# Kernel optimization log

Measured on AMD Instinct MI355X. Metric: run time of the kernel, lower is better.

## Reference

```python
import jax, jax.numpy as jnp
import numpy as np

N = 100000
E = 1600000
IN_FEATS = 128
H_FEATS = 64
BN_EPS = 1e-5


def setup_inputs() -> dict:
    key = jax.random.key(0)
    ks = jax.random.split(key, 8)
    features = jax.random.normal(ks[0], (N, IN_FEATS), dtype=jnp.float32)
    src = jax.random.randint(ks[1], (E,), 0, N, dtype=jnp.int32)
    dst = jax.random.randint(ks[2], (E,), 0, N, dtype=jnp.int32)
    # GraphConv weights (Glorot-ish scale) and biases
    W1 = jax.random.normal(ks[3], (IN_FEATS, H_FEATS), dtype=jnp.float32) / np.sqrt(IN_FEATS)
    b1 = jnp.zeros((H_FEATS,), dtype=jnp.float32)
    W2 = jax.random.normal(ks[4], (H_FEATS, H_FEATS), dtype=jnp.float32) / np.sqrt(H_FEATS)
    b2 = jnp.zeros((H_FEATS,), dtype=jnp.float32)
    gamma1 = jnp.ones((H_FEATS,), dtype=jnp.float32)
    beta1 = jnp.zeros((H_FEATS,), dtype=jnp.float32)
    gamma2 = jnp.ones((H_FEATS,), dtype=jnp.float32)
    beta2 = jnp.zeros((H_FEATS,), dtype=jnp.float32)
    return {"features": features, "W1": W1, "b1": b1, "gamma1": gamma1,
            "beta1": beta1, "W2": W2, "b2": b2, "gamma2": gamma2,
            "beta2": beta2, "src": src, "dst": dst}


def _degrees(src, dst):
    ones = jnp.ones((E,), dtype=jnp.float32)
    deg_out = jax.ops.segment_sum(ones, src, num_segments=N)
    deg_in = jax.ops.segment_sum(ones, dst, num_segments=N)
    # DGL clamps degree to >= 1 to avoid div by zero
    norm_src = jax.lax.rsqrt(jnp.maximum(deg_out, 1.0))  # [N]
    norm_dst = jax.lax.rsqrt(jnp.maximum(deg_in, 1.0))   # [N]
    return norm_src, norm_dst


def _graph_conv(x, W, b, src, dst, norm_src, norm_dst):
    # norm='both': D_out^{-1/2} scaling on src, sum-aggregate, D_in^{-1/2} on dst
    h = x * norm_src[:, None]          # [N, in]
    h = h @ W                          # [N, out] (transform before aggregate)
    msgs = h[src]                      # [E, out] gather
    agg = jax.ops.segment_sum(msgs, dst, num_segments=N)  # [N, out] scatter-add
    out = agg * norm_dst[:, None] + b
    return jax.nn.elu(out)


def _batch_norm(x, gamma, beta):
    mean = jnp.mean(x, axis=0)
    var = jnp.mean(jnp.square(x - mean), axis=0)
    return (x - mean) * jax.lax.rsqrt(var + BN_EPS) * gamma + beta


def reference(features, W1, b1, gamma1, beta1, W2, b2, gamma2, beta2, src, dst):
    # dropout p=0.0 (eval) -> identity
    norm_src, norm_dst = _degrees(src, dst)
    h1 = _graph_conv(features, W1, b1, src, dst, norm_src, norm_dst)
    h1 = _batch_norm(h1, gamma1, beta1)
    h2 = _graph_conv(h1, W2, b2, src, dst, norm_src, norm_dst)
    h2 = _batch_norm(h2, gamma2, beta2)
    return h2
```

## Files before the change

### kernel.cpp

```cpp
#include <hip/hip_runtime.h>
#include <cmath>

#define NFEAT_IN 128
#define NFEAT_H 64
#define BN_EPS 1e-5f
#define SCAP 2560

typedef unsigned short ushort_t;
typedef unsigned int uint_t;
typedef __attribute__((ext_vector_type(8))) short short8v;
typedef __attribute__((ext_vector_type(4))) float f32x4;

__device__ inline float b2f(ushort_t u) {
    return __uint_as_float(((uint_t)u) << 16);
}

__device__ inline ushort_t f2b(float f) {
    uint_t x = __float_as_uint(f);
    return (ushort_t)((x + 0x7FFFu + ((x >> 16) & 1u)) >> 16);
}


__global__ __launch_bounds__(256) void deg_s_kernel(const int* __restrict__ src,
                                                    int* __restrict__ deg_s, int E) {
    int i = blockIdx.x * 256 + threadIdx.x;
    if (i < E) atomicAdd(&deg_s[src[i]], 1);
}

__global__ __launch_bounds__(256) void dst_append_kernel(const int* __restrict__ src,
                                                         const int* __restrict__ dst,
                                                         int* __restrict__ curD,
                                                         uint_t* __restrict__ dbuf, int E) {
    int e = blockIdx.x * 256 + threadIdx.x;
    if (e < E) {
        int s = src[e], d = dst[e];
        int pD = atomicAdd(&curD[(d >> 7) * 16], 1);
        if (pD < SCAP) dbuf[(long long)(d >> 7) * SCAP + pD] = ((uint_t)s << 7) | (uint_t)(d & 127);
    }
}

__global__ __launch_bounds__(256) void bucket_hist_kernel(const uint_t* __restrict__ dbuf,
                                                          const int* __restrict__ curD,
                                                          int* __restrict__ deg_d, int N) {
    __shared__ int hist[128];
    int bb = blockIdx.x;
    int t = threadIdx.x;
    if (t < 128) hist[t] = 0;
    __syncthreads();
    int cnt = curD[bb * 16];
    if (cnt > SCAP) cnt = SCAP;
    long long base = (long long)bb * SCAP;
    for (int i = t; i < cnt; i += 256) atomicAdd(&hist[dbuf[base + i] & 127], 1);
    __syncthreads();
    if (t < 128) {
        int node = bb * 128 + t;
        if (node < N) deg_d[node] = hist[t];
    }
}

__global__ __launch_bounds__(256) void norm_scan_kernel(const int* __restrict__ deg_s,
                                                        const int* __restrict__ deg_d,
                                                        float* __restrict__ norm_s,
                                                        float* __restrict__ norm_d,
                                                        int* __restrict__ start,
                                                        int* __restrict__ counter,
                                                        float* __restrict__ stats, int N) {
    int tid = threadIdx.x;
    int i = blockIdx.x * 256 + tid;
    if (blockIdx.x == 0 && tid < 128) stats[tid] = 0.f;
    int lane = tid & 63, w = tid >> 6;
    int ds = 0, dd = 0;
    if (i < N) { ds = deg_s[i]; dd = deg_d[i]; }
    int pd = (dd + 7) & ~7;

    int x = pd;
#pragma unroll
    for (int off = 1; off < 64; off <<= 1) {
        int y = __shfl_up(x, off, 64);
        if (lane >= off) x += y;
    }
    __shared__ int wsum[4];
    __shared__ int blockbase;
    if (lane == 63) wsum[w] = x;
    __syncthreads();
    if (tid == 0)
        blockbase = atomicAdd(counter, wsum[0] + wsum[1] + wsum[2] + wsum[3]);
    __syncthreads();
    int base = blockbase;
    for (int ww = 0; ww < w; ++ww) base += wsum[ww];
    int st = base + x - pd;

    if (i < N) {
        norm_s[i] = rsqrtf((float)(ds > 1 ? ds : 1));
        norm_d[i] = rsqrtf((float)(dd > 1 ? dd : 1));
        start[i] = st;
    }
}

__global__ __launch_bounds__(256) void bucket_scatter_kernel(const uint_t* __restrict__ dbuf,
                                                             const int* __restrict__ curD,
                                                             const int* __restrict__ start,
                                                             int* __restrict__ col, int N) {
    __shared__ int cur[128];
    __shared__ int sst[128];
    int b = blockIdx.x, t = threadIdx.x;
    if (t < 128) {
        cur[t] = 0;
        int node = b * 128 + t;
        sst[t] = (node < N) ? start[node] : 0;
    }
    __syncthreads();
    int cnt = curD[b * 16];
    if (cnt > SCAP) cnt = SCAP;
    long long base = (long long)b * SCAP;
    for (int i = t; i < cnt; i += 256) {
        uint_t p = dbuf[base + i];
        int d0 = (int)(p & 127u);
        int s = (int)(p >> 7);
        int off = atomicAdd(&cur[d0], 1);
        col[sst[d0] + off] = s;
    }
}


__global__ __launch_bounds__(256) void gemm1_mfma(const float* __restrict__ x,
                                                  const float* __restrict__ W,
                                                  const float* __restrict__ norm,
                                                  ushort_t* __restrict__ out, int n) {
    constexpr int K = 128;
    __shared__ ushort_t sWh[64 * K];
    __shared__ ushort_t sWl[64 * K];
    int tid = threadIdx.x;
    for (int i = tid; i < K * 64; i += 256) {
        int k = i >> 6, f = i & 63;
        float v = W[i];
        ushort_t hi = f2b(v);
        ushort_t lo = f2b(v - b2f(hi));
        int idx = f * K + (((k >> 3) ^ (f & 7)) << 3) + (k & 7);
        sWh[idx] = hi;
        sWl[idx] = lo;
    }
    int w = tid >> 6, l = tid & 63, g = l >> 4;
    int rA = blockIdx.x * 64 + w * 16 + (l & 15);
    f32x4 acc[4];
#pragma unroll
    for (int nt = 0; nt < 4; ++nt) acc[nt] = (f32x4){0.f, 0.f, 0.f, 0.f};
    __syncthreads();

#pragma unroll
    for (int ks = 0; ks < K / 32; ++ks) {
        float av[8];
        if (rA < n) {
            const float* px = x + (long long)rA * K + ks * 32 + g * 8;
            float4 p0 = *(const float4*)px;
            float4 p1 = *(const float4*)(px + 4);
            av[0] = p0.x; av[1] = p0.y; av[2] = p0.z; av[3] = p0.w;
            av[4] = p1.x; av[5] = p1.y; av[6] = p1.z; av[7] = p1.w;
        } else {
#pragma unroll
            for (int j = 0; j < 8; ++j) av[j] = 0.f;
        }
        short8v ah, al;
#pragma unroll
        for (int j = 0; j < 8; ++j) {
            ushort_t h = f2b(av[j]);
            ah[j] = (short)h;
            al[j] = (short)f2b(av[j] - b2f(h));
        }
#pragma unroll
        for (int nt = 0; nt < 4; ++nt) {
            int f = nt * 16 + (l & 15);
            int c = (ks * 4 + g) ^ (f & 7);
            short8v bh = *(const short8v*)&sWh[f * K + (c << 3)];
            short8v bl = *(const short8v*)&sWl[f * K + (c << 3)];
            acc[nt] = __builtin_amdgcn_mfma_f32_16x16x32_bf16(ah, bh, acc[nt], 0, 0, 0);
            acc[nt] = __builtin_amdgcn_mfma_f32_16x16x32_bf16(ah, bl, acc[nt], 0, 0, 0);
            acc[nt] = __builtin_amdgcn_mfma_f32_16x16x32_bf16(al, bh, acc[nt], 0, 0, 0);
        }
    }
    int rb = blockIdx.x * 64 + w * 16 + g * 4;
    float nv[4];
#pragma unroll
    for (int j = 0; j < 4; ++j) {
        int r = rb + j;
        nv[j] = (r < n) ? norm[r] : 0.f;
    }
#pragma unroll
    for (int nt = 0; nt < 4; ++nt) {
        int cc = nt * 16 + (l & 15);
#pragma unroll
        for (int j = 0; j < 4; ++j) {
            int r = rb + j;
            if (r < n) out[(long long)r * 64 + cc] = f2b(acc[nt][j] * nv[j]);
        }
    }
}

__global__ __launch_bounds__(256) void gemm2_mfma(const ushort_t* __restrict__ x,
                                                  const float* __restrict__ W,
                                                  const float* __restrict__ coef,
                                                  const float* __restrict__ biasK,
                                                  const float* __restrict__ norm,
                                                  ushort_t* __restrict__ out, int n) {
    constexpr int K = 64;
    __shared__ ushort_t sWh[64 * K];
    __shared__ ushort_t sWl[64 * K];
    int tid = threadIdx.x;
    for (int i = tid; i < K * 64; i += 256) {
        int k = i >> 6, f = i & 63;
        float v = coef[k] * W[i];
        ushort_t hi = f2b(v);
        ushort_t lo = f2b(v - b2f(hi));
        int idx = f * K + (((k >> 3) ^ (f & 7)) << 3) + (k & 7);
        sWh[idx] = hi;
        sWl[idx] = lo;
    }
    int w = tid >> 6, l = tid & 63, g = l >> 4;
    int rA = blockIdx.x * 64 + w * 16 + (l & 15);
    f32x4 acc[4];
#pragma unroll
    for (int nt = 0; nt < 4; ++nt) acc[nt] = (f32x4){0.f, 0.f, 0.f, 0.f};
    __syncthreads();

#pragma unroll
    for (int ks = 0; ks < 2; ++ks) {
        short8v ah;
        if (rA < n) {
            uint4 u = *(const uint4*)(x + (long long)rA * 64 + ks * 32 + g * 8);
            union { uint4 u; short8v s; } cvt;
            cvt.u = u;
            ah = cvt.s;
        } else {
#pragma unroll
            for (int j = 0; j < 8; ++j) ah[j] = 0;
        }
#pragma unroll
        for (int nt = 0; nt < 4; ++nt) {
            int f = nt * 16 + (l & 15);
            int c = (ks * 4 + g) ^ (f & 7);
            short8v bh = *(const short8v*)&sWh[f * K + (c << 3)];
            short8v bl = *(const short8v*)&sWl[f * K + (c << 3)];
            acc[nt] = __builtin_amdgcn_mfma_f32_16x16x32_bf16(ah, bh, acc[nt], 0, 0, 0);
            acc[nt] = __builtin_amdgcn_mfma_f32_16x16x32_bf16(ah, bl, acc[nt], 0, 0, 0);
        }
    }
    int rb = blockIdx.x * 64 + w * 16 + g * 4;
    float nv[4];
#pragma unroll
    for (int j = 0; j < 4; ++j) {
        int r = rb + j;
        nv[j] = (r < n) ? norm[r] : 0.f;
    }
#pragma unroll
    for (int nt = 0; nt < 4; ++nt) {
        int cc = nt * 16 + (l & 15);
        float bk = biasK[cc];
#pragma unroll
        for (int j = 0; j < 4; ++j) {
            int r = rb + j;
            if (r < n) out[(long long)r * 64 + cc] = f2b((acc[nt][j] + bk) * nv[j]);
        }
    }
}

__global__ __launch_bounds__(256) void agg_fused_kernel(const ushort_t* __restrict__ h,
                                                        const int* __restrict__ start,
                                                        const int* __restrict__ degd,
                                                        const int* __restrict__ col,
                                                        const float* __restrict__ normd,
                                                        const float* __restrict__ bias,
                                                        ushort_t* __restrict__ outp,
                                                        float* __restrict__ stats, int N) {
    int tid = threadIdx.x;
    int w = tid >> 6;
    int lane = tid & 63;
    int g = lane >> 3;
    int j = lane & 7;

    float bb[8];
#pragma unroll
    for (int i = 0; i < 8; ++i) bb[i] = bias[j * 8 + i];

    float sum[8], sq[8];
#pragma unroll
    for (int i = 0; i < 8; ++i) { sum[i] = 0.f; sq[i] = 0.f; }

    for (int node = blockIdx.x * 4 + w; node < N; node += gridDim.x * 4) {
        int s0 = start[node];
        int d = degd[node];
        float acc[8];
#pragma unroll
        for (int i = 0; i < 8; ++i) acc[i] = 0.f;

        int k = 0;
        for (; k + 16 <= d; k += 16) {
            int c0 = col[s0 + k + g];
            int c1 = col[s0 + k + 8 + g];
            uint4 a = ((const uint4*)(h + (long long)c0 * 64))[j];
            uint4 b = ((const uint4*)(h + (long long)c1 * 64))[j];
            acc[0] += __uint_as_float(a.x << 16);
            acc[1] += __uint_as_float(a.x & 0xFFFF0000u);
            acc[2] += __uint_as_float(a.y << 16);
            acc[3] += __uint_as_float(a.y & 0xFFFF0000u);
            acc[4] += __uint_as_float(a.z << 16);
            acc[5] += __uint_as_float(a.z & 0xFFFF0000u);
            acc[6] += __uint_as_float(a.w << 16);
            acc[7] += __uint_as_float(a.w & 0xFFFF0000u);
            acc[0] += __uint_as_float(b.x << 16);
            acc[1] += __uint_as_float(b.x & 0xFFFF0000u);
            acc[2] += __uint_as_float(b.y << 16);
            acc[3] += __uint_as_float(b.y & 0xFFFF0000u);
            acc[4] += __uint_as_float(b.z << 16);
            acc[5] += __uint_as_float(b.z & 0xFFFF0000u);
            acc[6] += __uint_as_float(b.w << 16);
            acc[7] += __uint_as_float(b.w & 0xFFFF0000u);
        }
        for (; k + 8 <= d; k += 8) {
            int c0 = col[s0 + k + g];
            uint4 a = ((const uint4*)(h + (long long)c0 * 64))[j];
            acc[0] += __uint_as_float(a.x << 16);
            acc[1] += __uint_as_float(a.x & 0xFFFF0000u);
            acc[2] += __uint_as_float(a.y << 16);
            acc[3] += __uint_as_float(a.y & 0xFFFF0000u);
            acc[4] += __uint_as_float(a.z << 16);
            acc[5] += __uint_as_float(a.z & 0xFFFF0000u);
            acc[6] += __uint_as_float(a.w << 16);
            acc[7] += __uint_as_float(a.w & 0xFFFF0000u);
        }
        if (k < d) {
            int idx = k + g;
            if (idx < d) {
                int c0 = col[s0 + idx];
                uint4 a = ((const uint4*)(h + (long long)c0 * 64))[j];
                acc[0] += __uint_as_float(a.x << 16);
                acc[1] += __uint_as_float(a.x & 0xFFFF0000u);
                acc[2] += __uint_as_float(a.y << 16);
                acc[3] += __uint_as_float(a.y & 0xFFFF0000u);
                acc[4] += __uint_as_float(a.z << 16);
                acc[5] += __uint_as_float(a.z & 0xFFFF0000u);
                acc[6] += __uint_as_float(a.w << 16);
                acc[7] += __uint_as_float(a.w & 0xFFFF0000u);
            }
        }

#pragma unroll
        for (int i = 0; i < 8; ++i) {
            acc[i] += __shfl_xor(acc[i], 8, 64);
            acc[i] += __shfl_xor(acc[i], 16, 64);
            acc[i] += __shfl_xor(acc[i], 32, 64);
        }

        if (g == 0) {
            float nv = normd[node];
            float v[8];
#pragma unroll
            for (int i = 0; i < 8; ++i) {
                float t = acc[i] * nv + bb[i];
                t = t > 0.f ? t : expm1f(t);
                v[i] = t;
                sum[i] += t;
                sq[i] += t * t;
            }
            uint4 p;
            p.x = ((uint_t)f2b(v[1]) << 16) | f2b(v[0]);
            p.y = ((uint_t)f2b(v[3]) << 16) | f2b(v[2]);
            p.z = ((uint_t)f2b(v[5]) << 16) | f2b(v[4]);
            p.w = ((uint_t)f2b(v[7]) << 16) | f2b(v[6]);
            ((uint4*)(outp + (long long)node * 64))[j] = p;
        }
    }

    __shared__ float ssum[4][64];
    __shared__ float ssq[4][64];
    if (g == 0) {
#pragma unroll
        for (int i = 0; i < 8; ++i) {
            ssum[w][j * 8 + i] = sum[i];
            ssq[w][j * 8 + i] = sq[i];
        }
    }
    __syncthreads();
    if (tid < 64) {
        float s = ssum[0][tid] + ssum[1][tid] + ssum[2][tid] + ssum[3][tid];
        float q = ssq[0][tid] + ssq[1][tid] + ssq[2][tid] + ssq[3][tid];
        atomicAdd(&stats[tid], s);
        atomicAdd(&stats[64 + tid], q);
    }
}

__global__ __launch_bounds__(64) void bn_fin2_kernel(float* __restrict__ stats,
                                                     const float* __restrict__ gamma,
                                                     const float* __restrict__ beta,
                                                     const float* __restrict__ W2,
                                                     float* __restrict__ coef,
                                                     float* __restrict__ biasK, float inv_n) {
    int f = threadIdx.x;
    float mean = stats[f] * inv_n;
    float var = stats[64 + f] * inv_n - mean * mean;
    float a = gamma[f] * rsqrtf(var + BN_EPS);
    float cB = beta[f] - mean * a;
    coef[f] = a;
    coef[64 + f] = cB;
    stats[f] = 0.f;
    stats[64 + f] = 0.f;
    __shared__ float scB[64];
    scB[f] = cB;
    __syncthreads();
    float s = 0.f;
    for (int k = 0; k < 64; ++k) s = fmaf(scB[k], W2[k * 64 + f], s);
    biasK[f] = s;
}

__global__ __launch_bounds__(64) void bn_finalize(float* __restrict__ stats,
                                                  const float* __restrict__ gamma,
                                                  const float* __restrict__ beta,
                                                  float* __restrict__ coef, float inv_n) {
    int f = threadIdx.x;
    float mean = stats[f] * inv_n;
    float var = stats[64 + f] * inv_n - mean * mean;
    float a = gamma[f] * rsqrtf(var + BN_EPS);
    coef[f] = a;
    coef[64 + f] = beta[f] - mean * a;
}

__global__ __launch_bounds__(256) void bn_apply_b2f(const uint4* __restrict__ in,
                                                    const float* __restrict__ coef,
                                                    float4* __restrict__ out, long long n4) {
    long long i = (long long)blockIdx.x * 256 + threadIdx.x;
    if (i >= n4) return;
    int k = (int)((i & 7) << 3);
    uint4 u = in[i];
    float4 a, b;
    a.x = __uint_as_float(u.x << 16) * coef[k] + coef[64 + k];
    a.y = __uint_as_float(u.x & 0xFFFF0000u) * coef[k + 1] + coef[64 + k + 1];
    a.z = __uint_as_float(u.y << 16) * coef[k + 2] + coef[64 + k + 2];
    a.w = __uint_as_float(u.y & 0xFFFF0000u) * coef[k + 3] + coef[64 + k + 3];
    b.x = __uint_as_float(u.z << 16) * coef[k + 4] + coef[64 + k + 4];
    b.y = __uint_as_float(u.z & 0xFFFF0000u) * coef[k + 5] + coef[64 + k + 5];
    b.z = __uint_as_float(u.w << 16) * coef[k + 6] + coef[64 + k + 6];
    b.w = __uint_as_float(u.w & 0xFFFF0000u) * coef[k + 7] + coef[64 + k + 7];
    out[i * 2] = a;
    out[i * 2 + 1] = b;
}


extern "C" void kernel_launch(void* const* d_in, const int* in_sizes, int n_in,
                              void* d_out, int out_size, void* d_ws, size_t ws_size,
                              hipStream_t stream) {
    const float* features = (const float*)d_in[0];
    const float* W1 = (const float*)d_in[1];
    const float* b1 = (const float*)d_in[2];
    const float* gamma1 = (const float*)d_in[3];
    const float* beta1 = (const float*)d_in[4];
    const float* W2 = (const float*)d_in[5];
    const float* b2 = (const float*)d_in[6];
    const float* gamma2 = (const float*)d_in[7];
    const float* beta2 = (const float*)d_in[8];
    const int* src = (const int*)d_in[9];
    const int* dst = (const int*)d_in[10];
    int N = in_sizes[0] / NFEAT_IN;
    int E = in_sizes[9];

    float inv_n = 1.0f / (float)N;
    long long tot = (long long)N * 64;
    int eblk256 = (E + 255) / 256;
    int nblk256 = (N + 255) / 256;
    int NB = (N + 127) >> 7;
    int gblk = (N + 63) / 64;
    long long n4 = (long long)N * 8;
    int a4blk = (int)((n4 + 255) / 256);

    long long bufcap = (long long)NB * SCAP;
    long long colcap = (long long)E + 8LL * N;
    long long int_total = (16LL * NB + 4 + 3LL * N + bufcap + colcap + 3) & ~3LL;
    long long flt_count = ((2LL * N + 128 + 128 + 64) + 3) & ~3LL;

    int* ip = (int*)d_ws;
    int* curD = ip;
    int* counter = ip + 16LL * NB;
    int* deg_s = ip + 16LL * NB + 4;
    int* deg_d = deg_s + N;
    int* startv = deg_d + N;
    uint_t* dbuf = (uint_t*)(startv + N);
    int* col = (int*)(dbuf + bufcap);
    float* fp = (float*)(ip + int_total);
    float* norm_s = fp;
    float* norm_d = fp + N;
    float* stats = fp + 2LL * N;
    float* coef = stats + 128;
    float* biasK = coef + 128;
    ushort_t* hA = (ushort_t*)(fp + flt_count);
    ushort_t* oB = hA + tot;

    hipMemsetAsync(curD, 0, sizeof(int) * (16LL * NB + 4 + N), stream);
    deg_s_kernel<<<eblk256, 256, 0, stream>>>(src, deg_s, E);
    dst_append_kernel<<<eblk256, 256, 0, stream>>>(src, dst, curD, dbuf, E);
    bucket_hist_kernel<<<NB, 256, 0, stream>>>(dbuf, curD, deg_d, N);
    norm_scan_kernel<<<nblk256, 256, 0, stream>>>(deg_s, deg_d, norm_s, norm_d,
                                                  startv, counter, stats, N);
    bucket_scatter_kernel<<<NB, 256, 0, stream>>>(dbuf, curD, startv, col, N);

    gemm1_mfma<<<gblk, 256, 0, stream>>>(features, W1, norm_s, hA, N);
    agg_fused_kernel<<<2048, 256, 0, stream>>>(hA, startv, deg_d, col, norm_d, b1,
                                               oB, stats, N);
    bn_fin2_kernel<<<1, 64, 0, stream>>>(stats, gamma1, beta1, W2, coef, biasK, inv_n);

    gemm2_mfma<<<gblk, 256, 0, stream>>>(oB, W2, coef, biasK, norm_s, hA, N);
    agg_fused_kernel<<<2048, 256, 0, stream>>>(hA, startv, deg_d, col, norm_d, b2,
                                               oB, stats, N);
    bn_finalize<<<1, 64, 0, stream>>>(stats, gamma2, beta2, coef, inv_n);
    bn_apply_b2f<<<a4blk, 256, 0, stream>>>((const uint4*)oB, coef, (float4*)d_out, n4);
}
```

Baseline: 476.8 us.

## Split layer-1 aggregation into four source-range phases for gather cache locality

Edges in each destination's adjacency list are sorted into four groups by source-node quarter, with per-node group counts stored. Layer-1 aggregation then runs as four passes, each gathering only from one quarter of the feature table, so the working set of gathered rows fits better in cache. A separate finalize kernel applies normalization, bias, ELU and the BN statistics. The cost is extra passes that round-trip the accumulator through bf16 memory, which adds traffic and a rounding step per pass. The separate degree-count kernel is also fused into the append kernel.

```diff
diff --git a/kernel.cpp b/kernel.cpp
--- a/kernel.cpp
+++ b/kernel.cpp
@@ -21,19 +21,15 @@
 }
 
 
-__global__ __launch_bounds__(256) void deg_s_kernel(const int* __restrict__ src,
-                                                    int* __restrict__ deg_s, int E) {
-    int i = blockIdx.x * 256 + threadIdx.x;
-    if (i < E) atomicAdd(&deg_s[src[i]], 1);
-}
-
-__global__ __launch_bounds__(256) void dst_append_kernel(const int* __restrict__ src,
+__global__ __launch_bounds__(256) void deg_append_kernel(const int* __restrict__ src,
                                                          const int* __restrict__ dst,
+                                                         int* __restrict__ deg_s,
                                                          int* __restrict__ curD,
                                                          uint_t* __restrict__ dbuf, int E) {
     int e = blockIdx.x * 256 + threadIdx.x;
     if (e < E) {
         int s = src[e], d = dst[e];
+        atomicAdd(&deg_s[s], 1);
         int pD = atomicAdd(&curD[(d >> 7) * 16], 1);
         if (pD < SCAP) dbuf[(long long)(d >> 7) * SCAP + pD] = ((uint_t)s << 7) | (uint_t)(d & 127);
     }
@@ -97,28 +93,49 @@
     }
 }
 
-__global__ __launch_bounds__(256) void bucket_scatter_kernel(const uint_t* __restrict__ dbuf,
-                                                             const int* __restrict__ curD,
-                                                             const int* __restrict__ start,
-                                                             int* __restrict__ col, int N) {
-    __shared__ int cur[128];
-    __shared__ int sst[128];
+__global__ __launch_bounds__(256) void bucket_scatter2_kernel(const uint_t* __restrict__ dbuf,
+                                                              const int* __restrict__ curD,
+                                                              const int* __restrict__ start,
+                                                              int* __restrict__ col,
+                                                              uint2* __restrict__ rcnt,
+                                                              int N, int Q) {
+    __shared__ int cnt4[128][4];
+    __shared__ int cur[128][4];
     int b = blockIdx.x, t = threadIdx.x;
-    if (t < 128) {
-        cur[t] = 0;
-        int node = b * 128 + t;
-        sst[t] = (node < N) ? start[node] : 0;
-    }
+    if (t < 128) { cnt4[t][0] = 0; cnt4[t][1] = 0; cnt4[t][2] = 0; cnt4[t][3] = 0; }
     __syncthreads();
     int cnt = curD[b * 16];
     if (cnt > SCAP) cnt = SCAP;
     long long base = (long long)b * SCAP;
+    int Q2 = 2 * Q, Q3 = 3 * Q;
     for (int i = t; i < cnt; i += 256) {
         uint_t p = dbuf[base + i];
         int d0 = (int)(p & 127u);
         int s = (int)(p >> 7);
-        int off = atomicAdd(&cur[d0], 1);
-        col[sst[d0] + off] = s;
+        int r = (s >= Q) + (s >= Q2) + (s >= Q3);
+        atomicAdd(&cnt4[d0][r], 1);
+    }
+    __syncthreads();
+    if (t < 128) {
+        int node = b * 128 + t;
+        int st = (node < N) ? start[node] : 0;
+        int c0 = cnt4[t][0], c1 = cnt4[t][1], c2 = cnt4[t][2], c3 = cnt4[t][3];
+        cur[t][0] = st;
+        cur[t][1] = st + c0;
+        cur[t][2] = st + c0 + c1;
+        cur[t][3] = st + c0 + c1 + c2;
+        if (node < N)
+            rcnt[node] = make_uint2((uint_t)c0 | ((uint_t)c1 << 16),
+                                    (uint_t)c2 | ((uint_t)c3 << 16));
+    }
+    __syncthreads();
+    for (int i = t; i < cnt; i += 256) {
+        uint_t p = dbuf[base + i];
+        int d0 = (int)(p & 127u);
+        int s = (int)(p >> 7);
+        int r = (s >= Q) + (s >= Q2) + (s >= Q3);
+        int off = atomicAdd(&cur[d0][r], 1);
+        col[off] = s;
     }
 }
 
@@ -260,6 +277,123 @@
             int r = rb + j;
             if (r < n) out[(long long)r * 64 + cc] = f2b((acc[nt][j] + bk) * nv[j]);
         }
+    }
+}
+
+template <bool FIRST>
+__global__ __launch_bounds__(256) void agg_phase_kernel(const ushort_t* __restrict__ h,
+                                                        const int* __restrict__ start,
+                                                        const uint2* __restrict__ rcnt,
+                                                        const int* __restrict__ col,
+                                                        ushort_t* __restrict__ acc,
+                                                        int N, int r) {
+    int tid = threadIdx.x;
+    int w = tid >> 6;
+    int lane = tid & 63;
+    int g = lane >> 3;
+    int j = lane & 7;
+
+    for (int node = blockIdx.x * 4 + w; node < N; node += gridDim.x * 4) {
+        uint2 rc = rcnt[node];
+        int c0 = (int)(rc.x & 0xFFFFu), c1 = (int)(rc.x >> 16);
+        int c2 = (int)(rc.y & 0xFFFFu), c3 = (int)(rc.y >> 16);
+        int s0 = start[node];
+        int cnt;
+        if (r == 0) { cnt = c0; }
+        else if (r == 1) { s0 += c0; cnt = c1; }
+        else if (r == 2) { s0 += c0 + c1; cnt = c2; }
+        else { s0 += c0 + c1 + c2; cnt = c3; }
+        if (!FIRST && cnt == 0) continue;
+
+        float a8[8];
+#pragma unroll
+        for (int i = 0; i < 8; ++i) a8[i] = 0.f;
+
+        int k = 0;
+        for (; k + 8 <= cnt; k += 8) {
+            int c = col[s0 + k + g];
+            uint4 a = ((const uint4*)(h + (long long)c * 64))[j];
+            a8[0] += __uint_as_float(a.x << 16);
+            a8[1] += __uint_as_float(a.x & 0xFFFF0000u);
+            a8[2] += __uint_as_float(a.y << 16);
+            a8[3] += __uint_as_float(a.y & 0xFFFF0000u);
+            a8[4] += __uint_as_float(a.z << 16);
+            a8[5] += __uint_as_float(a.z & 0xFFFF0000u);
+            a8[6] += __uint_as_float(a.w << 16);
+            a8[7] += __uint_as_float(a.w & 0xFFFF0000u);
+        }
+        if (k < cnt) {
+            int idx = k + g;
+            if (idx < cnt) {
+                int c = col[s0 + idx];
+                uint4 a = ((const uint4*)(h + (long long)c * 64))[j];
+                a8[0] += __uint_as_float(a.x << 16);
+                a8[1] += __uint_as_float(a.x & 0xFFFF0000u);
+                a8[2] += __uint_as_float(a.y << 16);
+                a8[3] += __uint_as_float(a.y & 0xFFFF0000u);
+                a8[4] += __uint_as_float(a.z << 16);
+                a8[5] += __uint_as_float(a.z & 0xFFFF0000u);
+                a8[6] += __uint_as_float(a.w << 16);
+                a8[7] += __uint_as_float(a.w & 0xFFFF0000u);
+            }
+        }
+
+#pragma unroll
+        for (int i = 0; i < 8; ++i) {
+            a8[i] += __shfl_xor(a8[i], 8, 64);
+            a8[i] += __shfl_xor(a8[i], 16, 64);
+            a8[i] += __shfl_xor(a8[i], 32, 64);
+        }
+
+        if (g == 0) {
+            uint4* ap = (uint4*)(acc + (long long)node * 64) + j;
+            if (!FIRST) {
+                uint4 o = *ap;
+                a8[0] += __uint_as_float(o.x << 16);
+                a8[1] += __uint_as_float(o.x & 0xFFFF0000u);
+                a8[2] += __uint_as_float(o.y << 16);
+                a8[3] += __uint_as_float(o.y & 0xFFFF0000u);
+                a8[4] += __uint_as_float(o.z << 16);
+                a8[5] += __uint_as_float(o.z & 0xFFFF0000u);
+                a8[6] += __uint_as_float(o.w << 16);
+                a8[7] += __uint_as_float(o.w & 0xFFFF0000u);
+            }
+            uint4 p;
+            p.x = ((uint_t)f2b(a8[1]) << 16) | f2b(a8[0]);
+            p.y = ((uint_t)f2b(a8[3]) << 16) | f2b(a8[2]);
+            p.z = ((uint_t)f2b(a8[5]) << 16) | f2b(a8[4]);
+            p.w = ((uint_t)f2b(a8[7]) << 16) | f2b(a8[6]);
+            *ap = p;
+        }
+    }
+}
+
+__global__ __launch_bounds__(256) void finalize1_kernel(ushort_t* __restrict__ acc,
+                                                        const float* __restrict__ normd,
+                                                        const float* __restrict__ bias,
+                                                        float* __restrict__ stats, int N) {
+    int tid = threadIdx.x;
+    int f = tid & 63;
+    int w = tid >> 6;
+    float b = bias[f];
+    float sum = 0.f, sq = 0.f;
+    for (int node = blockIdx.x * 4 + w; node < N; node += gridDim.x * 4) {
+        long long i = (long long)node * 64 + f;
+        float v = b2f(acc[i]) * normd[node] + b;
+        v = v > 0.f ? v : expm1f(v);
+        acc[i] = f2b(v);
+        sum += v;
+        sq += v * v;
+    }
+    __shared__ float ssum[256], ssq[256];
+    ssum[tid] = sum;
+    ssq[tid] = sq;
+    __syncthreads();
+    if (tid < 64) {
+        float s = ssum[tid] + ssum[tid + 64] + ssum[tid + 128] + ssum[tid + 192];
+        float q = ssq[tid] + ssq[tid + 64] + ssq[tid + 128] + ssq[tid + 192];
+        atomicAdd(&stats[tid], s);
+        atomicAdd(&stats[64 + tid], q);
     }
 }
 
@@ -467,12 +601,13 @@
     int nblk256 = (N + 255) / 256;
     int NB = (N + 127) >> 7;
     int gblk = (N + 63) / 64;
+    int Q = (N + 3) / 4;
     long long n4 = (long long)N * 8;
     int a4blk = (int)((n4 + 255) / 256);
 
     long long bufcap = (long long)NB * SCAP;
     long long colcap = (long long)E + 8LL * N;
-    long long int_total = (16LL * NB + 4 + 3LL * N + bufcap + colcap + 3) & ~3LL;
+    long long int_total = (16LL * NB + 4 + 5LL * N + bufcap + colcap + 3) & ~3LL;
     long long flt_count = ((2LL * N + 128 + 128 + 64) + 3) & ~3LL;
 
     int* ip = (int*)d_ws;
@@ -481,7 +616,8 @@
     int* deg_s = ip + 16LL * NB + 4;
     int* deg_d = deg_s + N;
     int* startv = deg_d + N;
-    uint_t* dbuf = (uint_t*)(startv + N);
+    uint2* rcnt = (uint2*)(startv + N);
+    uint_t* dbuf = (uint_t*)(startv + N + 2LL * N);
     int* col = (int*)(dbuf + bufcap);
     float* fp = (float*)(ip + int_total);
     float* norm_s = fp;
@@ -493,16 +629,18 @@
     ushort_t* oB = hA + tot;
 
     hipMemsetAsync(curD, 0, sizeof(int) * (16LL * NB + 4 + N), stream);
-    deg_s_kernel<<<eblk256, 256, 0, stream>>>(src, deg_s, E);
-    dst_append_kernel<<<eblk256, 256, 0, stream>>>(src, dst, curD, dbuf, E);
+    deg_append_kernel<<<eblk256, 256, 0, stream>>>(src, dst, deg_s, curD, dbuf, E);
     bucket_hist_kernel<<<NB, 256, 0, stream>>>(dbuf, curD, deg_d, N);
     norm_scan_kernel<<<nblk256, 256, 0, stream>>>(deg_s, deg_d, norm_s, norm_d,
                                                   startv, counter, stats, N);
-    bucket_scatter_kernel<<<NB, 256, 0, stream>>>(dbuf, curD, startv, col, N);
+    bucket_scatter2_kernel<<<NB, 256, 0, stream>>>(dbuf, curD, startv, col, rcnt, N, Q);
 
     gemm1_mfma<<<gblk, 256, 0, stream>>>(features, W1, norm_s, hA, N);
-    agg_fused_kernel<<<2048, 256, 0, stream>>>(hA, startv, deg_d, col, norm_d, b1,
-                                               oB, stats, N);
+    agg_phase_kernel<true><<<2048, 256, 0, stream>>>(hA, startv, rcnt, col, oB, N, 0);
+    agg_phase_kernel<false><<<2048, 256, 0, stream>>>(hA, startv, rcnt, col, oB, N, 1);
+    agg_phase_kernel<false><<<2048, 256, 0, stream>>>(hA, startv, rcnt, col, oB, N, 2);
+    agg_phase_kernel<false><<<2048, 256, 0, stream>>>(hA, startv, rcnt, col, oB, N, 3);
+    finalize1_kernel<<<2048, 256, 0, stream>>>(oB, norm_d, b1, stats, N);
     bn_fin2_kernel<<<1, 64, 0, stream>>>(stats, gamma1, beta1, W2, coef, biasK, inv_n);
 
     gemm2_mfma<<<gblk, 256, 0, stream>>>(oB, W2, coef, biasK, norm_s, hA, N);
```

New measurement: 574.7 us. 20.5% more time.

## Fuse degree count into dst bucketing with block-local shared-memory reservation

Applied to the files above, without the earlier changes.

Merges the source-degree atomic pass into the destination bucketing kernel. Each block processes 4096 edges, builds a per-bucket histogram in shared memory, then reserves space in each global bucket with one atomic per bucket instead of one per edge. Positions inside a bucket come from shared-memory atomics. This cuts global atomic contention on the bucket counters and removes one launch and one read of src, at the cost of reading dst twice per block and running fewer, larger blocks.

```diff
diff --git a/kernel.cpp b/kernel.cpp
--- a/kernel.cpp
+++ b/kernel.cpp
@@ -5,6 +5,8 @@
 #define NFEAT_H 64
 #define BN_EPS 1e-5f
 #define SCAP 2560
+#define EPB 4096
+#define NBMAX 800
 
 typedef unsigned short ushort_t;
 typedef unsigned int uint_t;
@@ -21,19 +23,44 @@
 }
 
 
-__global__ __launch_bounds__(256) void deg_s_kernel(const int* __restrict__ src,
-                                                    int* __restrict__ deg_s, int E) {
-    int i = blockIdx.x * 256 + threadIdx.x;
-    if (i < E) atomicAdd(&deg_s[src[i]], 1);
-}
-
-__global__ __launch_bounds__(256) void dst_append_kernel(const int* __restrict__ src,
+__global__ __launch_bounds__(256) void block_append_kernel(const int* __restrict__ src,
+                                                           const int* __restrict__ dst,
+                                                           int* __restrict__ deg_s,
+                                                           int* __restrict__ curD,
+                                                           uint_t* __restrict__ dbuf,
+                                                           int E, int NB) {
+    __shared__ int lcnt[NBMAX];
+    __shared__ int lcur[NBMAX];
+    int t = threadIdx.x;
+    int e0 = blockIdx.x * EPB;
+    int e1 = min(e0 + EPB, E);
+    for (int i = t; i < NB; i += 256) lcnt[i] = 0;
+    __syncthreads();
+    for (int e = e0 + t; e < e1; e += 256)
+        atomicAdd(&lcnt[dst[e] >> 7], 1);
+    __syncthreads();
+    for (int i = t; i < NB; i += 256) {
+        int c = lcnt[i];
+        lcur[i] = (c > 0) ? atomicAdd(&curD[i * 16], c) : 0;
+    }
+    __syncthreads();
+    for (int e = e0 + t; e < e1; e += 256) {
+        int s = src[e], d = dst[e];
+        atomicAdd(&deg_s[s], 1);
+        int pos = atomicAdd(&lcur[d >> 7], 1);
+        if (pos < SCAP) dbuf[(long long)(d >> 7) * SCAP + pos] = ((uint_t)s << 7) | (uint_t)(d & 127);
+    }
+}
+
+__global__ __launch_bounds__(256) void deg_append_kernel(const int* __restrict__ src,
                                                          const int* __restrict__ dst,
+                                                         int* __restrict__ deg_s,
                                                          int* __restrict__ curD,
                                                          uint_t* __restrict__ dbuf, int E) {
     int e = blockIdx.x * 256 + threadIdx.x;
     if (e < E) {
         int s = src[e], d = dst[e];
+        atomicAdd(&deg_s[s], 1);
         int pD = atomicAdd(&curD[(d >> 7) * 16], 1);
         if (pD < SCAP) dbuf[(long long)(d >> 7) * SCAP + pD] = ((uint_t)s << 7) | (uint_t)(d & 127);
     }
@@ -493,8 +520,12 @@
     ushort_t* oB = hA + tot;
 
     hipMemsetAsync(curD, 0, sizeof(int) * (16LL * NB + 4 + N), stream);
-    deg_s_kernel<<<eblk256, 256, 0, stream>>>(src, deg_s, E);
-    dst_append_kernel<<<eblk256, 256, 0, stream>>>(src, dst, curD, dbuf, E);
+    if (NB <= NBMAX) {
+        int bblk = (E + EPB - 1) / EPB;
+        block_append_kernel<<<bblk, 256, 0, stream>>>(src, dst, deg_s, curD, dbuf, E, NB);
+    } else {
+        deg_append_kernel<<<eblk256, 256, 0, stream>>>(src, dst, deg_s, curD, dbuf, E);
+    }
     bucket_hist_kernel<<<NB, 256, 0, stream>>>(dbuf, curD, deg_d, N);
     norm_scan_kernel<<<nblk256, 256, 0, stream>>>(deg_s, deg_d, norm_s, norm_d,
                                                   startv, counter, stats, N);
```

Result: faster. 416.6 us (-12.6%).
